# Performance work log

Measured on AMD Instinct MI355X. Metric: run time of the kernel, lower is better.

Reference implementation:

```python
import jax, jax.numpy as jnp
import numpy as np

NEG = -9e15

def setup_inputs() -> dict:
    key = jax.random.key(0)
    k_h, k_adj, k_W, k_bW, k_a1, k_b1, k_a2, k_b2 = jax.random.split(key, 8)
    N, IN, OUT = 8192, 512, 512
    h = jax.random.normal(k_h, (N, IN), dtype=jnp.float32)
    adj = jax.random.randint(k_adj, (N, N), 0, 2, dtype=jnp.int32)
    # torch Linear default init: U(-1/sqrt(fan_in), 1/sqrt(fan_in))
    s_in = 1.0 / np.sqrt(IN)
    s_out = 1.0 / np.sqrt(OUT)
    W = jax.random.uniform(k_W, (IN, OUT), minval=-s_in, maxval=s_in, dtype=jnp.float32)
    bW = jax.random.uniform(k_bW, (OUT,), minval=-s_in, maxval=s_in, dtype=jnp.float32)
    a1 = jax.random.uniform(k_a1, (OUT,), minval=-s_out, maxval=s_out, dtype=jnp.float32)
    b1 = jax.random.uniform(k_b1, (), minval=-s_out, maxval=s_out, dtype=jnp.float32)
    a2 = jax.random.uniform(k_a2, (OUT,), minval=-s_out, maxval=s_out, dtype=jnp.float32)
    b2 = jax.random.uniform(k_b2, (), minval=-s_out, maxval=s_out, dtype=jnp.float32)
    return {"h": h, "adj": adj, "W": W, "bW": bW, "a1": a1, "b1": b1, "a2": a2, "b2": b2}

def reference(h, adj, W, bW, a1, b1, a2, b2):
    alpha = 0.2
    # Wh: [N, OUT]; dropout is identity at inference (training=False)
    Wh = h @ W + bW
    Wha1 = Wh @ a1 + b1  # [N]
    Wha2 = Wh @ a2 + b2  # [N]
    e = Wha1[:, None] + Wha2[None, :]  # [N, N] broadcast additive scores
    e = jnp.where(e > 0, e, alpha * e)  # leaky relu
    e = jnp.where(adj > 0, e, jnp.float32(-9e15))
    attention = jax.nn.softmax(e, axis=1)
    h_prime = attention @ Wh  # [N, OUT]
    return h_prime
```

## Files before the change

### kernel.cpp

```cpp
#include <hip/hip_runtime.h>
#include <hip/hip_bf16.h>
#include <stdint.h>


#define NN 8192
#define DD 512

typedef __attribute__((ext_vector_type(8))) short short8;
typedef __attribute__((ext_vector_type(8))) unsigned short ushort8;
typedef __attribute__((ext_vector_type(4))) float f32x4;
typedef __attribute__((ext_vector_type(4))) float float4v;
typedef __attribute__((ext_vector_type(4))) unsigned short ushort4v;

__device__ __forceinline__ uint16_t f2bf(float f) {
  union { float f; uint32_t u; } v; v.f = f;
  uint32_t u = v.u;
  u += 0x7fffu + ((u >> 16) & 1u);
  return (uint16_t)(u >> 16);
}

__device__ __forceinline__ uint32_t pk2bf(float lo, float hi) {
  union { __hip_bfloat162 h; uint32_t u; } v;
  v.h = __float22bfloat162_rn(make_float2(lo, hi));
  return v.u;
}

__device__ __forceinline__ void async_copy16(uint16_t* lds, const uint16_t* g) {
  __builtin_amdgcn_global_load_lds(
      (const __attribute__((address_space(1))) uint32_t*)g,
      (__attribute__((address_space(3))) uint32_t*)lds, 16, 0, 0);
}

__global__ __launch_bounds__(256) void conv_wt(const float* __restrict__ W,
                                               uint16_t* __restrict__ WT) {
  __shared__ float ts[64][65];
  int tid = threadIdx.x;
  int kt = (blockIdx.x >> 3) * 64, ct = (blockIdx.x & 7) * 64;
  #pragma unroll
  for (int it = 0; it < 4; ++it) {
    int idx = it * 256 + tid;
    int r = idx >> 4, q = idx & 15;
    float4v v = *(const float4v*)(W + (size_t)(kt + r) * 512 + ct + q * 4);
    ts[r][q * 4 + 0] = v.x; ts[r][q * 4 + 1] = v.y;
    ts[r][q * 4 + 2] = v.z; ts[r][q * 4 + 3] = v.w;
  }
  __syncthreads();
  #pragma unroll
  for (int it = 0; it < 4; ++it) {
    int idx = it * 256 + tid;
    int c = idx >> 4, q = idx & 15;
    ushort4v p;
    p.x = f2bf(ts[q * 4 + 0][c]); p.y = f2bf(ts[q * 4 + 1][c]);
    p.z = f2bf(ts[q * 4 + 2][c]); p.w = f2bf(ts[q * 4 + 3][c]);
    *(ushort4v*)(WT + (size_t)(ct + c) * 512 + kt + q * 4) = p;
  }
}

__global__ __launch_bounds__(512) void wh_gemm(const float* __restrict__ h,
                                               const uint16_t* __restrict__ WT,
                                               const float* __restrict__ bW,
                                               const float* __restrict__ a1,
                                               const float* __restrict__ a2,
                                               uint16_t* __restrict__ WhT,
                                               float* __restrict__ s1g,
                                               float* __restrict__ eb1g,
                                               float* __restrict__ eb2g) {
  __shared__ __align__(16) uint16_t At[32 * 32];
  __shared__ __align__(16) uint16_t Bt[512 * 32];
  __shared__ float s1loc[32], s2loc[32];
  int tid = threadIdx.x;
  int wave = tid >> 6, lane = tid & 63;
  int l15 = lane & 15, quad = lane >> 4;
  int i0 = blockIdx.x * 32;
  if (tid < 32) { s1loc[tid] = 0.f; s2loc[tid] = 0.f; }
  f32x4 acc[2][4] = {};
  for (int k0 = 0; k0 < 512; k0 += 32) {
    if (tid < 256) {
      int r = tid >> 3, ks = (tid & 7) * 4;
      float4v hv = *(const float4v*)(h + (size_t)(i0 + r) * 512 + k0 + ks);
      ushort4v p;
      p.x = f2bf(hv.x); p.y = f2bf(hv.y); p.z = f2bf(hv.z); p.w = f2bf(hv.w);
      *(ushort4v*)&At[r * 32 + ks] = p;
    }
    #pragma unroll
    for (int rr = 0; rr < 4; ++rr) {
      int idx = rr * 512 + tid;
      int c = idx >> 2, q = idx & 3;
      async_copy16(&Bt[idx * 8], WT + c * 512 + k0 + q * 8);
    }
    __syncthreads();
    short8 a0 = *(const short8*)&At[l15 * 32 + quad * 8];
    short8 a1f = *(const short8*)&At[(l15 + 16) * 32 + quad * 8];
    #pragma unroll
    for (int nt = 0; nt < 4; ++nt) {
      int c = wave * 64 + nt * 16 + l15;
      short8 b = *(const short8*)&Bt[c * 32 + quad * 8];
      acc[0][nt] = __builtin_amdgcn_mfma_f32_16x16x32_bf16(a0, b, acc[0][nt], 0, 0, 0);
      acc[1][nt] = __builtin_amdgcn_mfma_f32_16x16x32_bf16(a1f, b, acc[1][nt], 0, 0, 0);
    }
    __syncthreads();
  }
  #pragma unroll
  for (int mt = 0; mt < 2; ++mt) {
    int ib = i0 + mt * 16 + quad * 4;
    float r1[4] = {0.f, 0.f, 0.f, 0.f};
    float r2[4] = {0.f, 0.f, 0.f, 0.f};
    #pragma unroll
    for (int nt = 0; nt < 4; ++nt) {
      int c = wave * 64 + nt * 16 + l15;
      float bias = bW[c];
      float a1c = a1[c], a2c = a2[c];
      float v0 = acc[mt][nt].x + bias;
      float v1 = acc[mt][nt].y + bias;
      float v2 = acc[mt][nt].z + bias;
      float v3 = acc[mt][nt].w + bias;
      ushort4v p;
      p.x = f2bf(v0); p.y = f2bf(v1); p.z = f2bf(v2); p.w = f2bf(v3);
      *(ushort4v*)&WhT[(size_t)c * 8192 + ib] = p;
      r1[0] = fmaf(v0, a1c, r1[0]); r1[1] = fmaf(v1, a1c, r1[1]);
      r1[2] = fmaf(v2, a1c, r1[2]); r1[3] = fmaf(v3, a1c, r1[3]);
      r2[0] = fmaf(v0, a2c, r2[0]); r2[1] = fmaf(v1, a2c, r2[1]);
      r2[2] = fmaf(v2, a2c, r2[2]); r2[3] = fmaf(v3, a2c, r2[3]);
    }
    #pragma unroll
    for (int v = 0; v < 4; ++v) {
      int row = mt * 16 + quad * 4 + v;
      atomicAdd(&s1loc[row], r1[v]);
      atomicAdd(&s2loc[row], r2[v]);
    }
  }
  __syncthreads();
  if (tid < 32) {
    s1g[i0 + tid] = s1loc[tid];
    float v2 = s2loc[tid];
    eb1g[i0 + tid] = __expf(v2);
    eb2g[i0 + tid] = __expf(0.2f * v2);
  }
}

#define SCORE(aval, e1, e2, A1v, A2v, rs, dst)                       \
  { float m_ = fmaxf((A1v) * (e1), (A2v) * (e2));                    \
    m_ = ((aval) > 0) ? m_ : 0.f;                                    \
    (rs) += m_; (dst) = m_; }

__global__ __launch_bounds__(512, 4) void fused_attn(const int* __restrict__ adj,
                                                     const float* __restrict__ s1,
                                                     const float* __restrict__ b1,
                                                     const float* __restrict__ b2,
                                                     const float* __restrict__ eb1,
                                                     const float* __restrict__ eb2,
                                                     const uint16_t* __restrict__ WhT,
                                                     float* __restrict__ out) {
  __shared__ __align__(16) uint16_t At[64 * 128];
  __shared__ __align__(16) uint16_t Bt[128 * 128];
  __shared__ float sdv[64];
  int tid = threadIdx.x;
  int wave = tid >> 6, lane = tid & 63;
  int l15 = lane & 15, quad = lane >> 4;
  int kg = wave & 1, rg = (wave >> 1) & 1, cg = wave >> 2;
  int rb = blockIdx.x & 127, cb = blockIdx.x >> 7;
  int i0 = rb * 64, c0 = cb * 128;
  int r0 = tid >> 4, pp = tid & 15;
  int sc = pp ^ (r0 & 15);
  const int* arow0 = adj + (size_t)(i0 + r0) * NN + sc * 8;
  const int* arow1 = arow0 + (size_t)32 * NN;
  float bias = b1[0] + b2[0];
  float base0 = s1[i0 + r0] + bias;
  float base1 = s1[i0 + r0 + 32] + bias;
  float A10 = __expf(base0), A20 = __expf(0.2f * base0);
  float A11 = __expf(base1), A21 = __expf(0.2f * base1);
  float rsum0 = 0.f, rsum1 = 0.f;
  uint16_t* at0 = &At[(r0 * 16 + pp) * 8];
  uint16_t* at1 = &At[((r0 + 32) * 16 + pp) * 8];
  f32x4 acc[2][4] = {};
  for (int j0 = 0; j0 < NN; j0 += 128) {
    int4 a00 = *(const int4*)(arow0 + j0);
    int4 a01 = *(const int4*)(arow0 + j0 + 4);
    int4 a10 = *(const int4*)(arow1 + j0);
    int4 a11 = *(const int4*)(arow1 + j0 + 4);
    float4v e1v0 = *(const float4v*)(eb1 + j0 + sc * 8);
    float4v e1v1 = *(const float4v*)(eb1 + j0 + sc * 8 + 4);
    float4v e2v0 = *(const float4v*)(eb2 + j0 + sc * 8);
    float4v e2v1 = *(const float4v*)(eb2 + j0 + sc * 8 + 4);
    #pragma unroll
    for (int it = 0; it < 4; ++it) {
      int idx = it * 512 + tid;
      int r = idx >> 4, q = idx & 15;
      int bsc = q ^ (r & 15);
      async_copy16(&Bt[idx * 8], WhT + (size_t)(c0 + r) * NN + j0 + bsc * 8);
    }
    float t0[8], t1[8];
    SCORE(a00.x, e1v0.x, e2v0.x, A10, A20, rsum0, t0[0]);
    SCORE(a00.y, e1v0.y, e2v0.y, A10, A20, rsum0, t0[1]);
    SCORE(a00.z, e1v0.z, e2v0.z, A10, A20, rsum0, t0[2]);
    SCORE(a00.w, e1v0.w, e2v0.w, A10, A20, rsum0, t0[3]);
    SCORE(a01.x, e1v1.x, e2v1.x, A10, A20, rsum0, t0[4]);
    SCORE(a01.y, e1v1.y, e2v1.y, A10, A20, rsum0, t0[5]);
    SCORE(a01.z, e1v1.z, e2v1.z, A10, A20, rsum0, t0[6]);
    SCORE(a01.w, e1v1.w, e2v1.w, A10, A20, rsum0, t0[7]);
    SCORE(a10.x, e1v0.x, e2v0.x, A11, A21, rsum1, t1[0]);
    SCORE(a10.y, e1v0.y, e2v0.y, A11, A21, rsum1, t1[1]);
    SCORE(a10.z, e1v0.z, e2v0.z, A11, A21, rsum1, t1[2]);
    SCORE(a10.w, e1v0.w, e2v0.w, A11, A21, rsum1, t1[3]);
    SCORE(a11.x, e1v1.x, e2v1.x, A11, A21, rsum1, t1[4]);
    SCORE(a11.y, e1v1.y, e2v1.y, A11, A21, rsum1, t1[5]);
    SCORE(a11.z, e1v1.z, e2v1.z, A11, A21, rsum1, t1[6]);
    SCORE(a11.w, e1v1.w, e2v1.w, A11, A21, rsum1, t1[7]);
    ushort8 w0, w1;
    uint32_t* pw0 = (uint32_t*)&w0;
    uint32_t* pw1 = (uint32_t*)&w1;
    pw0[0] = pk2bf(t0[0], t0[1]); pw0[1] = pk2bf(t0[2], t0[3]);
    pw0[2] = pk2bf(t0[4], t0[5]); pw0[3] = pk2bf(t0[6], t0[7]);
    pw1[0] = pk2bf(t1[0], t1[1]); pw1[1] = pk2bf(t1[2], t1[3]);
    pw1[2] = pk2bf(t1[4], t1[5]); pw1[3] = pk2bf(t1[6], t1[7]);
    *(ushort8*)at0 = w0;
    *(ushort8*)at1 = w1;
    __syncthreads();
    #pragma unroll
    for (int kc = 0; kc < 2; ++kc) {
      int ch = kg * 8 + kc * 4 + quad;
      int ar0 = rg * 32 + l15, ar1 = ar0 + 16;
      short8 a0 = *(const short8*)&At[ar0 * 128 + ((ch ^ (ar0 & 15)) * 8)];
      short8 a1f = *(const short8*)&At[ar1 * 128 + ((ch ^ (ar1 & 15)) * 8)];
      #pragma unroll
      for (int ct = 0; ct < 4; ++ct) {
        int br = cg * 64 + ct * 16 + l15;
        short8 b = *(const short8*)&Bt[br * 128 + ((ch ^ (br & 15)) * 8)];
        acc[0][ct] = __builtin_amdgcn_mfma_f32_16x16x32_bf16(a0, b, acc[0][ct], 0, 0, 0);
        acc[1][ct] = __builtin_amdgcn_mfma_f32_16x16x32_bf16(a1f, b, acc[1][ct], 0, 0, 0);
      }
    }
    __syncthreads();
  }
  #pragma unroll
  for (int o = 1; o < 16; o <<= 1) {
    rsum0 += __shfl_xor(rsum0, o);
    rsum1 += __shfl_xor(rsum1, o);
  }
  if (pp == 0) {
    sdv[r0] = 1.0f / rsum0;
    sdv[r0 + 32] = 1.0f / rsum1;
  }
  float* red = (float*)Bt;
  int pid = rg * 2 + cg;
  if (kg == 1) {
    #pragma unroll
    for (int rt = 0; rt < 2; ++rt)
      #pragma unroll
      for (int ct = 0; ct < 4; ++ct)
        #pragma unroll
        for (int v = 0; v < 4; ++v)
          red[pid * 2048 + ((rt * 4 + ct) * 4 + v) * 64 + lane] = acc[rt][ct][v];
  }
  __syncthreads();
  if (kg == 0) {
    #pragma unroll
    for (int rt = 0; rt < 2; ++rt) {
      #pragma unroll
      for (int v = 0; v < 4; ++v) {
        int rloc = rg * 32 + rt * 16 + quad * 4 + v;
        float dv = sdv[rloc];
        #pragma unroll
        for (int ct = 0; ct < 4; ++ct) {
          float s = acc[rt][ct][v] + red[pid * 2048 + ((rt * 4 + ct) * 4 + v) * 64 + lane];
          out[(size_t)(i0 + rloc) * DD + c0 + cg * 64 + ct * 16 + l15] = s * dv;
        }
      }
    }
  }
}

extern "C" void kernel_launch(void* const* d_in, const int* in_sizes, int n_in,
                              void* d_out, int out_size, void* d_ws, size_t ws_size,
                              hipStream_t stream) {
  const float* h   = (const float*)d_in[0];
  const int*   adj = (const int*)d_in[1];
  const float* W   = (const float*)d_in[2];
  const float* bW  = (const float*)d_in[3];
  const float* a1  = (const float*)d_in[4];
  const float* b1  = (const float*)d_in[5];
  const float* a2  = (const float*)d_in[6];
  const float* b2  = (const float*)d_in[7];
  float* out = (float*)d_out;
  char* ws = (char*)d_ws;

  uint16_t* WhT = (uint16_t*)(ws);
  uint16_t* WT  = (uint16_t*)(ws + 8388608);
  float* s1     = (float*)(ws + 8912896);
  float* eb1    = (float*)(ws + 8945664);
  float* eb2    = (float*)(ws + 8978432);

  conv_wt<<<64, 256, 0, stream>>>(W, WT);
  wh_gemm<<<256, 512, 0, stream>>>(h, WT, bW, a1, a2, WhT, s1, eb1, eb2);
  fused_attn<<<512, 512, 0, stream>>>(adj, s1, b1, b2, eb1, eb2, WhT, out);
}
```

Before: 499.8 us.

## Double-buffer LDS tiles and prefetch next tiles in both GEMM kernels

Both the Wh GEMM and the fused attention kernel now use double-buffered shared-memory tiles. The next k/j tile's global loads and async copies are issued before the MFMA work on the current tile, and in the attention kernel the score computation for the next tile also overlaps with the MFMAs. The goal is to hide global-memory latency behind matrix math. The cost is doubled LDS for B (64KB for Bt in fused_attn), an extra barrier per iteration, and higher register pressure, all of which can lower occupancy under launch_bounds(512,4).

```diff
diff --git a/kernel.cpp b/kernel.cpp
--- a/kernel.cpp
+++ b/kernel.cpp
@@ -65,38 +65,57 @@
                                                float* __restrict__ s1g,
                                                float* __restrict__ eb1g,
                                                float* __restrict__ eb2g) {
-  __shared__ __align__(16) uint16_t At[32 * 32];
-  __shared__ __align__(16) uint16_t Bt[512 * 32];
+  __shared__ __align__(16) uint16_t At[2][32 * 32];
+  __shared__ __align__(16) uint16_t Bt[2][512 * 32];
   __shared__ float s1loc[32], s2loc[32];
   int tid = threadIdx.x;
   int wave = tid >> 6, lane = tid & 63;
   int l15 = lane & 15, quad = lane >> 4;
   int i0 = blockIdx.x * 32;
   if (tid < 32) { s1loc[tid] = 0.f; s2loc[tid] = 0.f; }
+  int ar = tid >> 3, aks = (tid & 7) * 4;
   f32x4 acc[2][4] = {};
-  for (int k0 = 0; k0 < 512; k0 += 32) {
-    if (tid < 256) {
-      int r = tid >> 3, ks = (tid & 7) * 4;
-      float4v hv = *(const float4v*)(h + (size_t)(i0 + r) * 512 + k0 + ks);
+  if (tid < 256) {
+    float4v hv = *(const float4v*)(h + (size_t)(i0 + ar) * 512 + aks);
+    ushort4v p;
+    p.x = f2bf(hv.x); p.y = f2bf(hv.y); p.z = f2bf(hv.z); p.w = f2bf(hv.w);
+    *(ushort4v*)&At[0][ar * 32 + aks] = p;
+  }
+  #pragma unroll
+  for (int rr = 0; rr < 4; ++rr) {
+    int idx = rr * 512 + tid;
+    int c = idx >> 2, q = idx & 3;
+    async_copy16(&Bt[0][idx * 8], WT + c * 512 + q * 8);
+  }
+  __syncthreads();
+  #pragma unroll 2
+  for (int kt = 0; kt < 16; ++kt) {
+    int cur = kt & 1;
+    int k0n = (kt + 1) * 32;
+    float4v hv;
+    if (kt < 15) {
+      if (tid < 256)
+        hv = *(const float4v*)(h + (size_t)(i0 + ar) * 512 + k0n + aks);
+      #pragma unroll
+      for (int rr = 0; rr < 4; ++rr) {
+        int idx = rr * 512 + tid;
+        int c = idx >> 2, q = idx & 3;
+        async_copy16(&Bt[cur ^ 1][idx * 8], WT + c * 512 + k0n + q * 8);
+      }
+    }
+    short8 a0 = *(const short8*)&At[cur][l15 * 32 + quad * 8];
+    short8 a1f = *(const short8*)&At[cur][(l15 + 16) * 32 + quad * 8];
+    #pragma unroll
+    for (int nt = 0; nt < 4; ++nt) {
+      int c = wave * 64 + nt * 16 + l15;
+      short8 b = *(const short8*)&Bt[cur][c * 32 + quad * 8];
+      acc[0][nt] = __builtin_amdgcn_mfma_f32_16x16x32_bf16(a0, b, acc[0][nt], 0, 0, 0);
+      acc[1][nt] = __builtin_amdgcn_mfma_f32_16x16x32_bf16(a1f, b, acc[1][nt], 0, 0, 0);
+    }
+    if (kt < 15 && tid < 256) {
       ushort4v p;
       p.x = f2bf(hv.x); p.y = f2bf(hv.y); p.z = f2bf(hv.z); p.w = f2bf(hv.w);
-      *(ushort4v*)&At[r * 32 + ks] = p;
-    }
-    #pragma unroll
-    for (int rr = 0; rr < 4; ++rr) {
-      int idx = rr * 512 + tid;
-      int c = idx >> 2, q = idx & 3;
-      async_copy16(&Bt[idx * 8], WT + c * 512 + k0 + q * 8);
-    }
-    __syncthreads();
-    short8 a0 = *(const short8*)&At[l15 * 32 + quad * 8];
-    short8 a1f = *(const short8*)&At[(l15 + 16) * 32 + quad * 8];
-    #pragma unroll
-    for (int nt = 0; nt < 4; ++nt) {
-      int c = wave * 64 + nt * 16 + l15;
-      short8 b = *(const short8*)&Bt[c * 32 + quad * 8];
-      acc[0][nt] = __builtin_amdgcn_mfma_f32_16x16x32_bf16(a0, b, acc[0][nt], 0, 0, 0);
-      acc[1][nt] = __builtin_amdgcn_mfma_f32_16x16x32_bf16(a1f, b, acc[1][nt], 0, 0, 0);
+      *(ushort4v*)&At[cur ^ 1][ar * 32 + aks] = p;
     }
     __syncthreads();
   }
@@ -143,6 +162,41 @@
     m_ = ((aval) > 0) ? m_ : 0.f;                                    \
     (rs) += m_; (dst) = m_; }
 
+#define SCOREPACK()                                                  \
+  { float t0[8], t1[8];                                              \
+    SCORE(a00.x, e1v0.x, e2v0.x, A10, A20, rsum0, t0[0]);            \
+    SCORE(a00.y, e1v0.y, e2v0.y, A10, A20, rsum0, t0[1]);            \
+    SCORE(a00.z, e1v0.z, e2v0.z, A10, A20, rsum0, t0[2]);            \
+    SCORE(a00.w, e1v0.w, e2v0.w, A10, A20, rsum0, t0[3]);            \
+    SCORE(a01.x, e1v1.x, e2v1.x, A10, A20, rsum0, t0[4]);            \
+    SCORE(a01.y, e1v1.y, e2v1.y, A10, A20, rsum0, t0[5]);            \
+    SCORE(a01.z, e1v1.z, e2v1.z, A10, A20, rsum0, t0[6]);            \
+    SCORE(a01.w, e1v1.w, e2v1.w, A10, A20, rsum0, t0[7]);            \
+    SCORE(a10.x, e1v0.x, e2v0.x, A11, A21, rsum1, t1[0]);            \
+    SCORE(a10.y, e1v0.y, e2v0.y, A11, A21, rsum1, t1[1]);            \
+    SCORE(a10.z, e1v0.z, e2v0.z, A11, A21, rsum1, t1[2]);            \
+    SCORE(a10.w, e1v0.w, e2v0.w, A11, A21, rsum1, t1[3]);            \
+    SCORE(a11.x, e1v1.x, e2v1.x, A11, A21, rsum1, t1[4]);            \
+    SCORE(a11.y, e1v1.y, e2v1.y, A11, A21, rsum1, t1[5]);            \
+    SCORE(a11.z, e1v1.z, e2v1.z, A11, A21, rsum1, t1[6]);            \
+    SCORE(a11.w, e1v1.w, e2v1.w, A11, A21, rsum1, t1[7]);            \
+    uint32_t* pw0 = (uint32_t*)&w0;                                  \
+    uint32_t* pw1 = (uint32_t*)&w1;                                  \
+    pw0[0] = pk2bf(t0[0], t0[1]); pw0[1] = pk2bf(t0[2], t0[3]);      \
+    pw0[2] = pk2bf(t0[4], t0[5]); pw0[3] = pk2bf(t0[6], t0[7]);      \
+    pw1[0] = pk2bf(t1[0], t1[1]); pw1[1] = pk2bf(t1[2], t1[3]);      \
+    pw1[2] = pk2bf(t1[4], t1[5]); pw1[3] = pk2bf(t1[6], t1[7]); }
+
+#define LOADA(j0_)                                                   \
+  a00 = *(const int4*)(arow0 + (j0_));                               \
+  a01 = *(const int4*)(arow0 + (j0_) + 4);                           \
+  a10 = *(const int4*)(arow1 + (j0_));                               \
+  a11 = *(const int4*)(arow1 + (j0_) + 4);                           \
+  e1v0 = *(const float4v*)(eb1 + (j0_) + sc * 8);                    \
+  e1v1 = *(const float4v*)(eb1 + (j0_) + sc * 8 + 4);                \
+  e2v0 = *(const float4v*)(eb2 + (j0_) + sc * 8);                    \
+  e2v1 = *(const float4v*)(eb2 + (j0_) + sc * 8 + 4);
+
 __global__ __launch_bounds__(512, 4) void fused_attn(const int* __restrict__ adj,
                                                      const float* __restrict__ s1,
                                                      const float* __restrict__ b1,
@@ -152,8 +206,7 @@
                                                      const uint16_t* __restrict__ WhT,
                                                      float* __restrict__ out) {
   __shared__ __align__(16) uint16_t At[64 * 128];
-  __shared__ __align__(16) uint16_t Bt[128 * 128];
-  __shared__ float sdv[64];
+  __shared__ __align__(16) uint16_t Bt[2][128 * 128];
   int tid = threadIdx.x;
   int wave = tid >> 6, lane = tid & 63;
   int l15 = lane & 15, quad = lane >> 4;
@@ -173,49 +226,38 @@
   uint16_t* at0 = &At[(r0 * 16 + pp) * 8];
   uint16_t* at1 = &At[((r0 + 32) * 16 + pp) * 8];
   f32x4 acc[2][4] = {};
-  for (int j0 = 0; j0 < NN; j0 += 128) {
-    int4 a00 = *(const int4*)(arow0 + j0);
-    int4 a01 = *(const int4*)(arow0 + j0 + 4);
-    int4 a10 = *(const int4*)(arow1 + j0);
-    int4 a11 = *(const int4*)(arow1 + j0 + 4);
-    float4v e1v0 = *(const float4v*)(eb1 + j0 + sc * 8);
-    float4v e1v1 = *(const float4v*)(eb1 + j0 + sc * 8 + 4);
-    float4v e2v0 = *(const float4v*)(eb2 + j0 + sc * 8);
-    float4v e2v1 = *(const float4v*)(eb2 + j0 + sc * 8 + 4);
-    #pragma unroll
-    for (int it = 0; it < 4; ++it) {
-      int idx = it * 512 + tid;
-      int r = idx >> 4, q = idx & 15;
-      int bsc = q ^ (r & 15);
-      async_copy16(&Bt[idx * 8], WhT + (size_t)(c0 + r) * NN + j0 + bsc * 8);
-    }
-    float t0[8], t1[8];
-    SCORE(a00.x, e1v0.x, e2v0.x, A10, A20, rsum0, t0[0]);
-    SCORE(a00.y, e1v0.y, e2v0.y, A10, A20, rsum0, t0[1]);
-    SCORE(a00.z, e1v0.z, e2v0.z, A10, A20, rsum0, t0[2]);
-    SCORE(a00.w, e1v0.w, e2v0.w, A10, A20, rsum0, t0[3]);
-    SCORE(a01.x, e1v1.x, e2v1.x, A10, A20, rsum0, t0[4]);
-    SCORE(a01.y, e1v1.y, e2v1.y, A10, A20, rsum0, t0[5]);
-    SCORE(a01.z, e1v1.z, e2v1.z, A10, A20, rsum0, t0[6]);
-    SCORE(a01.w, e1v1.w, e2v1.w, A10, A20, rsum0, t0[7]);
-    SCORE(a10.x, e1v0.x, e2v0.x, A11, A21, rsum1, t1[0]);
-    SCORE(a10.y, e1v0.y, e2v0.y, A11, A21, rsum1, t1[1]);
-    SCORE(a10.z, e1v0.z, e2v0.z, A11, A21, rsum1, t1[2]);
-    SCORE(a10.w, e1v0.w, e2v0.w, A11, A21, rsum1, t1[3]);
-    SCORE(a11.x, e1v1.x, e2v1.x, A11, A21, rsum1, t1[4]);
-    SCORE(a11.y, e1v1.y, e2v1.y, A11, A21, rsum1, t1[5]);
-    SCORE(a11.z, e1v1.z, e2v1.z, A11, A21, rsum1, t1[6]);
-    SCORE(a11.w, e1v1.w, e2v1.w, A11, A21, rsum1, t1[7]);
-    ushort8 w0, w1;
-    uint32_t* pw0 = (uint32_t*)&w0;
-    uint32_t* pw1 = (uint32_t*)&w1;
-    pw0[0] = pk2bf(t0[0], t0[1]); pw0[1] = pk2bf(t0[2], t0[3]);
-    pw0[2] = pk2bf(t0[4], t0[5]); pw0[3] = pk2bf(t0[6], t0[7]);
-    pw1[0] = pk2bf(t1[0], t1[1]); pw1[1] = pk2bf(t1[2], t1[3]);
-    pw1[2] = pk2bf(t1[4], t1[5]); pw1[3] = pk2bf(t1[6], t1[7]);
-    *(ushort8*)at0 = w0;
-    *(ushort8*)at1 = w1;
-    __syncthreads();
+  int4 a00, a01, a10, a11;
+  float4v e1v0, e1v1, e2v0, e2v1;
+  ushort8 w0, w1;
+
+  LOADA(0);
+  #pragma unroll
+  for (int bi = 0; bi < 4; ++bi) {
+    int idx = bi * 512 + tid;
+    int r = idx >> 4, q = idx & 15;
+    int bsc = q ^ (r & 15);
+    async_copy16(&Bt[0][idx * 8], WhT + (size_t)(c0 + r) * NN + bsc * 8);
+  }
+  SCOREPACK();
+  *(ushort8*)at0 = w0;
+  *(ushort8*)at1 = w1;
+  __syncthreads();
+
+  #pragma unroll 2
+  for (int it = 0; it < 64; ++it) {
+    int cur = it & 1;
+    int j0n = (it + 1) << 7;
+    if (it < 63) {
+      LOADA(j0n);
+      #pragma unroll
+      for (int bi = 0; bi < 4; ++bi) {
+        int idx = bi * 512 + tid;
+        int r = idx >> 4, q = idx & 15;
+        int bsc = q ^ (r & 15);
+        async_copy16(&Bt[cur ^ 1][idx * 8],
+                     WhT + (size_t)(c0 + r) * NN + j0n + bsc * 8);
+      }
+    }
     #pragma unroll
     for (int kc = 0; kc < 2; ++kc) {
       int ch = kg * 8 + kc * 4 + quad;
@@ -225,23 +267,31 @@
       #pragma unroll
       for (int ct = 0; ct < 4; ++ct) {
         int br = cg * 64 + ct * 16 + l15;
-        short8 b = *(const short8*)&Bt[br * 128 + ((ch ^ (br & 15)) * 8)];
+        short8 b = *(const short8*)&Bt[cur][br * 128 + ((ch ^ (br & 15)) * 8)];
         acc[0][ct] = __builtin_amdgcn_mfma_f32_16x16x32_bf16(a0, b, acc[0][ct], 0, 0, 0);
         acc[1][ct] = __builtin_amdgcn_mfma_f32_16x16x32_bf16(a1f, b, acc[1][ct], 0, 0, 0);
       }
     }
+    if (it < 63) SCOREPACK();
     __syncthreads();
-  }
+    if (it < 63) {
+      *(ushort8*)at0 = w0;
+      *(ushort8*)at1 = w1;
+    }
+    __syncthreads();
+  }
+
   #pragma unroll
   for (int o = 1; o < 16; o <<= 1) {
     rsum0 += __shfl_xor(rsum0, o);
     rsum1 += __shfl_xor(rsum1, o);
   }
+  float* sdv = (float*)At;
   if (pp == 0) {
     sdv[r0] = 1.0f / rsum0;
     sdv[r0 + 32] = 1.0f / rsum1;
   }
-  float* red = (float*)Bt;
+  float* red = (float*)&Bt[0][0];
   int pid = rg * 2 + cg;
   if (kg == 1) {
     #pragma unroll
```

After: 546.7 us. 9.4% more time.

## Pack adjacency into a bitmask before the fused attention kernel

Applied to the files above, without the earlier changes.

Adds a prepass kernel that reads the int32 adjacency matrix once and uses a wave ballot to write a one-bit-per-entry mask. The fused attention kernel then reads one mask byte per eight columns instead of eight int32 values. Each adjacency row was previously reread by every column-block of the output, so this aims to cut that repeated large global-memory traffic. In exchange it adds an extra launch, a full pass over adj, and an 8 MB workspace buffer.

```diff
diff --git a/kernel.cpp b/kernel.cpp
--- a/kernel.cpp
+++ b/kernel.cpp
@@ -29,6 +29,18 @@
   __builtin_amdgcn_global_load_lds(
       (const __attribute__((address_space(1))) uint32_t*)g,
       (__attribute__((address_space(3))) uint32_t*)lds, 16, 0, 0);
+}
+
+__global__ __launch_bounds__(256) void maskbuild(const int* __restrict__ adj,
+                                                 unsigned long long* __restrict__ mask) {
+  int g = blockIdx.x * 256 + threadIdx.x;
+  #pragma unroll 4
+  for (int it = 0; it < 128; ++it) {
+    size_t e = (size_t)it * 524288 + g;
+    int a = adj[e];
+    unsigned long long m = __ballot(a > 0);
+    if ((threadIdx.x & 63) == 0) mask[e >> 6] = m;
+  }
 }
 
 __global__ __launch_bounds__(256) void conv_wt(const float* __restrict__ W,
@@ -138,12 +150,12 @@
   }
 }
 
-#define SCORE(aval, e1, e2, A1v, A2v, rs, dst)                       \
+#define SCOREB(mv, k, e1, e2, A1v, A2v, rs, dst)                     \
   { float m_ = fmaxf((A1v) * (e1), (A2v) * (e2));                    \
-    m_ = ((aval) > 0) ? m_ : 0.f;                                    \
+    m_ = ((mv) & (1u << (k))) ? m_ : 0.f;                            \
     (rs) += m_; (dst) = m_; }
 
-__global__ __launch_bounds__(512, 4) void fused_attn(const int* __restrict__ adj,
+__global__ __launch_bounds__(512, 4) void fused_attn(const unsigned char* __restrict__ mask,
                                                      const float* __restrict__ s1,
                                                      const float* __restrict__ b1,
                                                      const float* __restrict__ b2,
@@ -162,8 +174,8 @@
   int i0 = rb * 64, c0 = cb * 128;
   int r0 = tid >> 4, pp = tid & 15;
   int sc = pp ^ (r0 & 15);
-  const int* arow0 = adj + (size_t)(i0 + r0) * NN + sc * 8;
-  const int* arow1 = arow0 + (size_t)32 * NN;
+  const unsigned char* mrow0 = mask + (size_t)(i0 + r0) * 1024 + sc;
+  const unsigned char* mrow1 = mrow0 + (size_t)32 * 1024;
   float bias = b1[0] + b2[0];
   float base0 = s1[i0 + r0] + bias;
   float base1 = s1[i0 + r0 + 32] + bias;
@@ -174,10 +186,8 @@
   uint16_t* at1 = &At[((r0 + 32) * 16 + pp) * 8];
   f32x4 acc[2][4] = {};
   for (int j0 = 0; j0 < NN; j0 += 128) {
-    int4 a00 = *(const int4*)(arow0 + j0);
-    int4 a01 = *(const int4*)(arow0 + j0 + 4);
-    int4 a10 = *(const int4*)(arow1 + j0);
-    int4 a11 = *(const int4*)(arow1 + j0 + 4);
+    uint32_t mb0 = mrow0[j0 >> 3];
+    uint32_t mb1 = mrow1[j0 >> 3];
     float4v e1v0 = *(const float4v*)(eb1 + j0 + sc * 8);
     float4v e1v1 = *(const float4v*)(eb1 + j0 + sc * 8 + 4);
     float4v e2v0 = *(const float4v*)(eb2 + j0 + sc * 8);
@@ -190,22 +200,22 @@
       async_copy16(&Bt[idx * 8], WhT + (size_t)(c0 + r) * NN + j0 + bsc * 8);
     }
     float t0[8], t1[8];
-    SCORE(a00.x, e1v0.x, e2v0.x, A10, A20, rsum0, t0[0]);
-    SCORE(a00.y, e1v0.y, e2v0.y, A10, A20, rsum0, t0[1]);
-    SCORE(a00.z, e1v0.z, e2v0.z, A10, A20, rsum0, t0[2]);
-    SCORE(a00.w, e1v0.w, e2v0.w, A10, A20, rsum0, t0[3]);
-    SCORE(a01.x, e1v1.x, e2v1.x, A10, A20, rsum0, t0[4]);
-    SCORE(a01.y, e1v1.y, e2v1.y, A10, A20, rsum0, t0[5]);
-    SCORE(a01.z, e1v1.z, e2v1.z, A10, A20, rsum0, t0[6]);
-    SCORE(a01.w, e1v1.w, e2v1.w, A10, A20, rsum0, t0[7]);
-    SCORE(a10.x, e1v0.x, e2v0.x, A11, A21, rsum1, t1[0]);
-    SCORE(a10.y, e1v0.y, e2v0.y, A11, A21, rsum1, t1[1]);
-    SCORE(a10.z, e1v0.z, e2v0.z, A11, A21, rsum1, t1[2]);
-    SCORE(a10.w, e1v0.w, e2v0.w, A11, A21, rsum1, t1[3]);
-    SCORE(a11.x, e1v1.x, e2v1.x, A11, A21, rsum1, t1[4]);
-    SCORE(a11.y, e1v1.y, e2v1.y, A11, A21, rsum1, t1[5]);
-    SCORE(a11.z, e1v1.z, e2v1.z, A11, A21, rsum1, t1[6]);
-    SCORE(a11.w, e1v1.w, e2v1.w, A11, A21, rsum1, t1[7]);
+    SCOREB(mb0, 0, e1v0.x, e2v0.x, A10, A20, rsum0, t0[0]);
+    SCOREB(mb0, 1, e1v0.y, e2v0.y, A10, A20, rsum0, t0[1]);
+    SCOREB(mb0, 2, e1v0.z, e2v0.z, A10, A20, rsum0, t0[2]);
+    SCOREB(mb0, 3, e1v0.w, e2v0.w, A10, A20, rsum0, t0[3]);
+    SCOREB(mb0, 4, e1v1.x, e2v1.x, A10, A20, rsum0, t0[4]);
+    SCOREB(mb0, 5, e1v1.y, e2v1.y, A10, A20, rsum0, t0[5]);
+    SCOREB(mb0, 6, e1v1.z, e2v1.z, A10, A20, rsum0, t0[6]);
+    SCOREB(mb0, 7, e1v1.w, e2v1.w, A10, A20, rsum0, t0[7]);
+    SCOREB(mb1, 0, e1v0.x, e2v0.x, A11, A21, rsum1, t1[0]);
+    SCOREB(mb1, 1, e1v0.y, e2v0.y, A11, A21, rsum1, t1[1]);
+    SCOREB(mb1, 2, e1v0.z, e2v0.z, A11, A21, rsum1, t1[2]);
+    SCOREB(mb1, 3, e1v0.w, e2v0.w, A11, A21, rsum1, t1[3]);
+    SCOREB(mb1, 4, e1v1.x, e2v1.x, A11, A21, rsum1, t1[4]);
+    SCOREB(mb1, 5, e1v1.y, e2v1.y, A11, A21, rsum1, t1[5]);
+    SCOREB(mb1, 6, e1v1.z, e2v1.z, A11, A21, rsum1, t1[6]);
+    SCOREB(mb1, 7, e1v1.w, e2v1.w, A11, A21, rsum1, t1[7]);
     ushort8 w0, w1;
     uint32_t* pw0 = (uint32_t*)&w0;
     uint32_t* pw1 = (uint32_t*)&w1;
@@ -289,8 +299,11 @@
   float* s1     = (float*)(ws + 8912896);
   float* eb1    = (float*)(ws + 8945664);
   float* eb2    = (float*)(ws + 8978432);
-
+  unsigned long long* mask = (unsigned long long*)(ws + 9011200);
+
+  maskbuild<<<2048, 256, 0, stream>>>(adj, mask);
   conv_wt<<<64, 256, 0, stream>>>(W, WT);
   wh_gemm<<<256, 512, 0, stream>>>(h, WT, bW, a1, a2, WhT, s1, eb1, eb2);
-  fused_attn<<<512, 512, 0, stream>>>(adj, s1, b1, b2, eb1, eb2, WhT, out);
-}
+  fused_attn<<<512, 512, 0, stream>>>((const unsigned char*)mask, s1, b1, b2,
+                                      eb1, eb2, WhT, out);
+}
```

Result: slower. 562.8 us (+12.6%).

## Split attention key dimension across two blocks and combine partial sums

Applied to the files above, without the earlier changes.

Adds a split-K variant of the fused attention kernel: each block handles half of the neighbor columns, writes unnormalized partial outputs and partial row sums to workspace, and a new combine kernel sums the halves and normalizes. This doubles the grid from 512 to 1024 blocks to fill more CUs, and raises the launch-bounds occupancy hint from 4 to 6. The cost is writing and rereading two full 8192x512 fp32 partial buffers, plus an extra launch. The original path is kept as a fallback when the workspace is too small.

```diff
diff --git a/kernel.cpp b/kernel.cpp
--- a/kernel.cpp
+++ b/kernel.cpp
@@ -143,13 +143,16 @@
     m_ = ((aval) > 0) ? m_ : 0.f;                                    \
     (rs) += m_; (dst) = m_; }
 
-__global__ __launch_bounds__(512, 4) void fused_attn(const int* __restrict__ adj,
+template<bool SPLIT>
+__global__ __launch_bounds__(512, 6) void fused_attn(const int* __restrict__ adj,
                                                      const float* __restrict__ s1,
                                                      const float* __restrict__ b1,
                                                      const float* __restrict__ b2,
                                                      const float* __restrict__ eb1,
                                                      const float* __restrict__ eb2,
                                                      const uint16_t* __restrict__ WhT,
+                                                     float* __restrict__ Pp,
+                                                     float* __restrict__ dpart,
                                                      float* __restrict__ out) {
   __shared__ __align__(16) uint16_t At[64 * 128];
   __shared__ __align__(16) uint16_t Bt[128 * 128];
@@ -158,8 +161,12 @@
   int wave = tid >> 6, lane = tid & 63;
   int l15 = lane & 15, quad = lane >> 4;
   int kg = wave & 1, rg = (wave >> 1) & 1, cg = wave >> 2;
-  int rb = blockIdx.x & 127, cb = blockIdx.x >> 7;
+  int bid = blockIdx.x;
+  int rb = bid & 127, cb = (bid >> 7) & 3;
+  int js = SPLIT ? (bid >> 9) : 0;
   int i0 = rb * 64, c0 = cb * 128;
+  int jbase = js * 4096;
+  int niter = SPLIT ? 32 : 64;
   int r0 = tid >> 4, pp = tid & 15;
   int sc = pp ^ (r0 & 15);
   const int* arow0 = adj + (size_t)(i0 + r0) * NN + sc * 8;
@@ -173,7 +180,8 @@
   uint16_t* at0 = &At[(r0 * 16 + pp) * 8];
   uint16_t* at1 = &At[((r0 + 32) * 16 + pp) * 8];
   f32x4 acc[2][4] = {};
-  for (int j0 = 0; j0 < NN; j0 += 128) {
+  for (int it = 0; it < niter; ++it) {
+    int j0 = jbase + it * 128;
     int4 a00 = *(const int4*)(arow0 + j0);
     int4 a01 = *(const int4*)(arow0 + j0 + 4);
     int4 a10 = *(const int4*)(arow1 + j0);
@@ -183,8 +191,8 @@
     float4v e2v0 = *(const float4v*)(eb2 + j0 + sc * 8);
     float4v e2v1 = *(const float4v*)(eb2 + j0 + sc * 8 + 4);
     #pragma unroll
-    for (int it = 0; it < 4; ++it) {
-      int idx = it * 512 + tid;
+    for (int bi = 0; bi < 4; ++bi) {
+      int idx = bi * 512 + tid;
       int r = idx >> 4, q = idx & 15;
       int bsc = q ^ (r & 15);
       async_copy16(&Bt[idx * 8], WhT + (size_t)(c0 + r) * NN + j0 + bsc * 8);
@@ -237,12 +245,20 @@
     rsum0 += __shfl_xor(rsum0, o);
     rsum1 += __shfl_xor(rsum1, o);
   }
-  if (pp == 0) {
-    sdv[r0] = 1.0f / rsum0;
-    sdv[r0 + 32] = 1.0f / rsum1;
+  if (SPLIT) {
+    if (pp == 0 && cb == 0) {
+      dpart[js * NN + i0 + r0] = rsum0;
+      dpart[js * NN + i0 + r0 + 32] = rsum1;
+    }
+  } else {
+    if (pp == 0) {
+      sdv[r0] = 1.0f / rsum0;
+      sdv[r0 + 32] = 1.0f / rsum1;
+    }
   }
   float* red = (float*)Bt;
   int pid = rg * 2 + cg;
+  __syncthreads();
   if (kg == 1) {
     #pragma unroll
     for (int rt = 0; rt < 2; ++rt)
@@ -259,15 +275,33 @@
       #pragma unroll
       for (int v = 0; v < 4; ++v) {
         int rloc = rg * 32 + rt * 16 + quad * 4 + v;
-        float dv = sdv[rloc];
+        float dv = SPLIT ? 1.0f : sdv[rloc];
         #pragma unroll
         for (int ct = 0; ct < 4; ++ct) {
           float s = acc[rt][ct][v] + red[pid * 2048 + ((rt * 4 + ct) * 4 + v) * 64 + lane];
-          out[(size_t)(i0 + rloc) * DD + c0 + cg * 64 + ct * 16 + l15] = s * dv;
+          size_t o = (size_t)(i0 + rloc) * DD + c0 + cg * 64 + ct * 16 + l15;
+          if (SPLIT) Pp[(size_t)js * NN * DD + o] = s;
+          else out[o] = s * dv;
         }
       }
     }
   }
+}
+
+__global__ __launch_bounds__(256) void combine(const float* __restrict__ Pp,
+                                               const float* __restrict__ dpart,
+                                               float* __restrict__ out) {
+  int idx = blockIdx.x * 256 + threadIdx.x;
+  int i = idx >> 7;
+  float4v p0 = *(const float4v*)(Pp + (size_t)idx * 4);
+  float4v p1 = *(const float4v*)(Pp + (size_t)NN * DD + (size_t)idx * 4);
+  float dv = 1.0f / (dpart[i] + dpart[NN + i]);
+  float4v o;
+  o.x = (p0.x + p1.x) * dv;
+  o.y = (p0.y + p1.y) * dv;
+  o.z = (p0.z + p1.z) * dv;
+  o.w = (p0.w + p1.w) * dv;
+  *(float4v*)(out + (size_t)idx * 4) = o;
 }
 
 extern "C" void kernel_launch(void* const* d_in, const int* in_sizes, int n_in,
@@ -289,8 +323,18 @@
   float* s1     = (float*)(ws + 8912896);
   float* eb1    = (float*)(ws + 8945664);
   float* eb2    = (float*)(ws + 8978432);
+  float* Pp     = (float*)(ws + 9011200);
+  float* dpart  = (float*)(ws + 42565632);
+  const size_t NEED = 42631168ULL;
 
   conv_wt<<<64, 256, 0, stream>>>(W, WT);
   wh_gemm<<<256, 512, 0, stream>>>(h, WT, bW, a1, a2, WhT, s1, eb1, eb2);
-  fused_attn<<<512, 512, 0, stream>>>(adj, s1, b1, b2, eb1, eb2, WhT, out);
-}
+  if (ws_size >= NEED) {
+    fused_attn<true><<<1024, 512, 0, stream>>>(adj, s1, b1, b2, eb1, eb2,
+                                               WhT, Pp, dpart, out);
+    combine<<<4096, 256, 0, stream>>>(Pp, dpart, out);
+  } else {
+    fused_attn<false><<<512, 512, 0, stream>>>(adj, s1, b1, b2, eb1, eb2,
+                                               WhT, Pp, dpart, out);
+  }
+}
```

Result: slower. 795.4 us (+59.2%).
